# Performance work log

Measured on AMD Instinct MI355X. Metric: run time of the kernel, lower is better.

The kernel has to match this reference:

```python
import jax, jax.numpy as jnp
import numpy as np

LN_EPS = 1e-5


def _sage_mean(x, Wl, bl, src, dst, ew, n_nodes):
    # lin_l then gather-weight-scatter mean: out[i] = mean_{j->i} ew * (x[j] @ Wl + bl)
    h = x @ Wl + bl                                  # [N, D]
    msg = h[src] * ew[:, None]                       # [E, D] gather + scale
    s = jax.ops.segment_sum(msg, dst, num_segments=n_nodes)          # [N, D]
    cnt = jax.ops.segment_sum(jnp.ones_like(ew), dst, num_segments=n_nodes)
    return s / jnp.maximum(cnt, 1.0)[:, None]


def _layernorm(x, gamma, beta):
    mu = jnp.mean(x, axis=-1, keepdims=True)
    var = jnp.var(x, axis=-1, keepdims=True)
    return (x - mu) * jax.lax.rsqrt(var + LN_EPS) * gamma + beta


def setup_inputs() -> dict:
    key = jax.random.key(0)
    ks = jax.random.split(key, 8)
    N, E, D = 50000, 800000, 128
    x = jax.random.normal(ks[0], (N, D), dtype=jnp.float32)
    edge_index = jax.random.randint(ks[1], (2, E), 0, N, dtype=jnp.int64)
    edge_weight = jax.random.uniform(ks[2], (E,), dtype=jnp.float32)
    sc = 1.0 / np.sqrt(D)
    Wl1 = jax.random.normal(ks[3], (D, D), dtype=jnp.float32) * sc
    bl1 = jnp.zeros((D,), dtype=jnp.float32)
    Wl2 = jax.random.normal(ks[4], (D, D), dtype=jnp.float32) * sc
    bl2 = jnp.zeros((D,), dtype=jnp.float32)
    gamma = jnp.ones((D,), dtype=jnp.float32)
    beta = jnp.zeros((D,), dtype=jnp.float32)
    return {"x": x, "edge_index": edge_index, "edge_weight": edge_weight,
            "Wl1": Wl1, "bl1": bl1, "Wl2": Wl2, "bl2": bl2,
            "gamma": gamma, "beta": beta}


def reference(x, edge_index, edge_weight, Wl1, bl1, Wl2, bl2, gamma, beta):
    N = x.shape[0]
    src, dst = edge_index[0], edge_index[1]
    # Layer 1: WeightedSAGEConv (no self-loops; update() returns aggr only)
    x1 = _sage_mean(x, Wl1, bl1, src, dst, edge_weight, N)
    # Layer 2: ResGraphConv — residual is Identity (in==out), add self-loops w=1
    loops = jnp.arange(N, dtype=edge_index.dtype)
    src2 = jnp.concatenate([src, loops])
    dst2 = jnp.concatenate([dst, loops])
    ew2 = jnp.concatenate([edge_weight, jnp.ones((N,), dtype=edge_weight.dtype)])
    out = _sage_mean(x1, Wl2, bl2, src2, dst2, ew2, N)
    out = _layernorm(out + x1, gamma, beta)
    return jax.nn.gelu(out, approximate=False)
```

## Files before the change

kernel.cpp:

```cpp
#include <hip/hip_runtime.h>
#include <math.h>

#define DF 128
#define NPB 256
#define EPB 4096
#define CAP 7168

typedef __attribute__((ext_vector_type(8))) short bf16x8;
typedef __attribute__((ext_vector_type(4))) float f32x4;

__device__ __forceinline__ float bf2f(uint u) {
    union { uint i; float f; } v; v.i = u << 16; return v.f;
}
__device__ __forceinline__ uint f2bf(float f) {
    union { float f; uint i; } v; v.f = f;
    return (v.i + 0x7fffu + ((v.i >> 16) & 1u)) >> 16;
}


__global__ void prep_k(const float* __restrict__ x, uint* __restrict__ xb, int n4,
                       const float* __restrict__ W1, const float* __restrict__ W2,
                       uint* __restrict__ Wt1, uint* __restrict__ Wt2,
                       const int* __restrict__ dst, int* __restrict__ bhist, int E,
                       int cvtxB) {
    __shared__ int lh[256];
    int b = blockIdx.x;
    int t = threadIdx.x;
    if (b < cvtxB) {
        int i = b * 256 + t;
        if (i < n4) {
            float4 v = ((const float4*)x)[i];
            uint2 o;
            o.x = f2bf(v.x) | (f2bf(v.y) << 16);
            o.y = f2bf(v.z) | (f2bf(v.w) << 16);
            ((uint2*)xb)[i] = o;
        }
    } else if (b < cvtxB + 64) {
        int i = (b - cvtxB) * 256 + t;
        const float* W = (i < 8192) ? W1 : W2;
        uint* Wt = (i < 8192) ? Wt1 : Wt2;
        int j = i & 8191;
        int n = j >> 6, kk = j & 63;
        Wt[n * 64 + kk] = f2bf(W[(2 * kk) * DF + n]) | (f2bf(W[(2 * kk + 1) * DF + n]) << 16);
    } else {
        int hb = b - cvtxB - 64;
        int base = hb * EPB;
        lh[t] = 0;
        __syncthreads();
#pragma unroll
        for (int k = 0; k < EPB / 256; ++k) {
            int i = base + k * 256 + t;
            if (i < E) atomicAdd(&lh[dst[i] >> 8], 1);
        }
        __syncthreads();
        bhist[hb * 256 + t] = lh[t];
    }
}

__global__ void bscan_k(const int* __restrict__ bhist, int histB,
                        int* __restrict__ bkoff, int* __restrict__ gcur) {
    int t = threadIdx.x;
    int v = 0;
#pragma unroll 4
    for (int hb = 0; hb < histB; ++hb) v += bhist[hb * 256 + t];
    __shared__ int sm[256];
    sm[t] = v;
    __syncthreads();
    for (int off = 1; off < 256; off <<= 1) {
        int u = (t >= off) ? sm[t - off] : 0;
        __syncthreads();
        sm[t] += u;
        __syncthreads();
    }
    int ex = sm[t] - v;
    bkoff[t] = ex;
    gcur[t] = ex;
    if (t == 255) bkoff[256] = sm[255];
}

__global__ __launch_bounds__(256) void passA_k(
    const int* __restrict__ src, const int* __restrict__ dst,
    const float* __restrict__ ew, int* __restrict__ gcur,
    uint2* __restrict__ stage, int E) {
    __shared__ int lhist[256];
    __shared__ int lscan[256];
    __shared__ int lcur[256];
    __shared__ int gbase[256];
    __shared__ unsigned char lbk[EPB];
    __shared__ uint2 img[EPB];
    int t = threadIdx.x;
    int base = blockIdx.x * EPB;
    int cnt = min(EPB, E - base);
    lhist[t] = 0;
    __syncthreads();
    uint ps[16], pw[16];
    int pb[16];
#pragma unroll
    for (int k = 0; k < 16; ++k) {
        int i = base + k * 256 + t;
        pb[k] = -1;
        if (i < E) {
            int d = dst[i];
            int bk = d >> 8;
            pb[k] = bk;
            ps[k] = (uint)src[i] | ((uint)(d & 255) << 23);
            pw[k] = __float_as_uint(ew[i]);
            atomicAdd(&lhist[bk], 1);
        }
    }
    __syncthreads();
    int v = lhist[t];
    lscan[t] = v;
    __syncthreads();
    for (int off = 1; off < 256; off <<= 1) {
        int u = (t >= off) ? lscan[t - off] : 0;
        __syncthreads();
        lscan[t] += u;
        __syncthreads();
    }
    lcur[t] = lscan[t] - v;
    if (v > 0) gbase[t] = atomicAdd(&gcur[t], v);
    __syncthreads();
#pragma unroll
    for (int k = 0; k < 16; ++k) {
        if (pb[k] >= 0) {
            int p = atomicAdd(&lcur[pb[k]], 1);
            img[p] = make_uint2(ps[k], pw[k]);
            lbk[p] = (unsigned char)pb[k];
        }
    }
    __syncthreads();
    for (int i = t; i < cnt; i += 256) {
        int bk = lbk[i];
        stage[gbase[bk] + (i - (lscan[bk] - lhist[bk]))] = img[i];
    }
}

__global__ __launch_bounds__(256) void passB_k(
    const uint2* __restrict__ stage, const int* __restrict__ bkoff,
    int* __restrict__ rowptr, int* __restrict__ cursor,
    int2* __restrict__ adj, int N, int nbk) {
    __shared__ int lhist[256];
    __shared__ int lpre[256];
    __shared__ int lcur[256];
    __shared__ uint2 img[CAP];
    int t = threadIdx.x;
    int b = blockIdx.x;
    int nb0 = b * NPB;
    int nn = min(NPB, N - nb0);
    int ebase = bkoff[b];
    int ecnt = bkoff[b + 1] - ebase;
    lhist[t] = 0;
    __syncthreads();
    for (int i = t; i < ecnt; i += 256) {
        uint2 e = stage[ebase + i];
        atomicAdd(&lhist[(e.x >> 23) & 255], 1);
    }
    __syncthreads();
    int v = lhist[t];
    lpre[t] = v;
    __syncthreads();
    for (int off = 1; off < 256; off <<= 1) {
        int u = (t >= off) ? lpre[t - off] : 0;
        __syncthreads();
        lpre[t] += u;
        __syncthreads();
    }
    int myoff = lpre[t] - v;
    lcur[t] = myoff;
    if (t < nn) {
        rowptr[nb0 + t] = ebase + myoff;
        cursor[nb0 + t] = ebase + myoff;
    }
    if (b == nbk - 1 && t == 0) rowptr[N] = ebase + ecnt;
    __syncthreads();
    if (ecnt <= CAP) {
        for (int i = t; i < ecnt; i += 256) {
            uint2 e = stage[ebase + i];
            int p = atomicAdd(&lcur[(e.x >> 23) & 255], 1);
            img[p] = make_uint2(e.x & 0x7fffffu, e.y);
        }
        __syncthreads();
        for (int i = t; i < ecnt; i += 256) {
            uint2 e = img[i];
            adj[ebase + i] = make_int2((int)e.x, (int)e.y);
        }
    } else {
        for (int i = t; i < ecnt; i += 256) {
            uint2 e = stage[ebase + i];
            int dl = (e.x >> 23) & 255;
            int p = atomicAdd(&cursor[nb0 + dl], 1);
            adj[p] = make_int2((int)(e.x & 0x7fffffu), (int)e.y);
        }
    }
}


__global__ void histn_k(const int* __restrict__ dst, int* __restrict__ cnt, int E) {
    int i = blockIdx.x * blockDim.x + threadIdx.x;
    if (i < E) atomicAdd(&cnt[dst[i]], 1);
}

__global__ void partial_k(const int* __restrict__ cnt, int* __restrict__ bsum, int N) {
    int t = threadIdx.x, b = blockIdx.x;
    int base = b * 1024 + t * 4;
    int s = 0;
    if (base + 4 <= N) {
        int4 v = *(const int4*)(cnt + base);
        s = v.x + v.y + v.z + v.w;
    } else {
        for (int j = 0; j < 4; ++j)
            if (base + j < N) s += cnt[base + j];
    }
    __shared__ int sm[256];
    sm[t] = s;
    __syncthreads();
    for (int off = 128; off > 0; off >>= 1) {
        if (t < off) sm[t] += sm[t + off];
        __syncthreads();
    }
    if (t == 0) bsum[b] = sm[0];
}

__global__ void scanb_k(const int* __restrict__ bsum, int* __restrict__ boff,
                        int* __restrict__ rowptr, int nb, int N) {
    int t = threadIdx.x;
    int v = (t < nb) ? bsum[t] : 0;
    __shared__ int sm[256];
    sm[t] = v;
    __syncthreads();
    for (int off = 1; off < 256; off <<= 1) {
        int u = (t >= off) ? sm[t - off] : 0;
        __syncthreads();
        sm[t] += u;
        __syncthreads();
    }
    if (t < nb) boff[t] = sm[t] - v;
    if (t == 255) rowptr[N] = sm[255];
}

__global__ void rowfill_k(const int* __restrict__ cnt, const int* __restrict__ boff,
                          int* __restrict__ rowptr, int* __restrict__ cursor, int N) {
    int t = threadIdx.x, b = blockIdx.x;
    int base = b * 1024 + t * 4;
    int c0 = 0, c1 = 0, c2 = 0, c3 = 0;
    if (base + 4 <= N) {
        int4 v = *(const int4*)(cnt + base);
        c0 = v.x; c1 = v.y; c2 = v.z; c3 = v.w;
    } else {
        if (base + 0 < N) c0 = cnt[base + 0];
        if (base + 1 < N) c1 = cnt[base + 1];
        if (base + 2 < N) c2 = cnt[base + 2];
        if (base + 3 < N) c3 = cnt[base + 3];
    }
    int s = c0 + c1 + c2 + c3;
    __shared__ int sm[256];
    sm[t] = s;
    __syncthreads();
    for (int off = 1; off < 256; off <<= 1) {
        int u = (t >= off) ? sm[t - off] : 0;
        __syncthreads();
        sm[t] += u;
        __syncthreads();
    }
    int run = boff[b] + sm[t] - s;
    if (base + 0 < N) { rowptr[base + 0] = run; cursor[base + 0] = run; run += c0; }
    if (base + 1 < N) { rowptr[base + 1] = run; cursor[base + 1] = run; run += c1; }
    if (base + 2 < N) { rowptr[base + 2] = run; cursor[base + 2] = run; run += c2; }
    if (base + 3 < N) { rowptr[base + 3] = run; cursor[base + 3] = run; run += c3; }
}

__global__ void fill_k(const int* __restrict__ src, const int* __restrict__ dst,
                       const float* __restrict__ ew, int* __restrict__ cursor,
                       int2* __restrict__ adj, int E) {
    int i = blockIdx.x * blockDim.x + threadIdx.x;
    if (i < E) {
        int p = atomicAdd(&cursor[dst[i]], 1);
        int2 e;
        e.x = src[i];
        e.y = __float_as_int(ew[i]);
        adj[p] = e;
    }
}


template <int SELF>
__global__ void agg_k(const uint2* __restrict__ xb2, const int* __restrict__ rowptr,
                      const int2* __restrict__ adj, uint2* __restrict__ aggb2,
                      float* __restrict__ sumew, int N) {
    int wid = (blockIdx.x * blockDim.x + threadIdx.x) >> 6;
    int lane = threadIdx.x & 63;
    if (wid >= N) return;
    int half = lane >> 5;
    int sl = lane & 31;
    int lo = rowptr[wid], hi = rowptr[wid + 1];
    float a0 = 0.f, a1 = 0.f, a2 = 0.f, a3 = 0.f, ws = 0.f;
    if (SELF && half == 0) {
        uint2 v = xb2[(size_t)wid * 32 + sl];
        a0 = bf2f(v.x & 0xffffu); a1 = bf2f(v.x >> 16);
        a2 = bf2f(v.y & 0xffffu); a3 = bf2f(v.y >> 16);
    }
    for (int base = lo; base < hi; base += 64) {
        int p = base + lane;
        int sidx = 0; float wv = 0.f;
        if (p < hi) {
            int2 e = adj[p];
            sidx = e.x;
            wv = __int_as_float(e.y);
        }
        ws += wv;
        int cnt = min(hi - base, 64);
        int j = 0;
        for (; j + 8 <= cnt; j += 8) {
            int s0 = __shfl(sidx, j + half),     s1 = __shfl(sidx, j + 2 + half);
            int s2 = __shfl(sidx, j + 4 + half), s3 = __shfl(sidx, j + 6 + half);
            float w0 = __shfl(wv, j + half),     w1 = __shfl(wv, j + 2 + half);
            float w2 = __shfl(wv, j + 4 + half), w3 = __shfl(wv, j + 6 + half);
            uint2 v0 = xb2[(size_t)s0 * 32 + sl];
            uint2 v1 = xb2[(size_t)s1 * 32 + sl];
            uint2 v2 = xb2[(size_t)s2 * 32 + sl];
            uint2 v3 = xb2[(size_t)s3 * 32 + sl];
            a0 += w0 * bf2f(v0.x & 0xffffu); a1 += w0 * bf2f(v0.x >> 16);
            a2 += w0 * bf2f(v0.y & 0xffffu); a3 += w0 * bf2f(v0.y >> 16);
            a0 += w1 * bf2f(v1.x & 0xffffu); a1 += w1 * bf2f(v1.x >> 16);
            a2 += w1 * bf2f(v1.y & 0xffffu); a3 += w1 * bf2f(v1.y >> 16);
            a0 += w2 * bf2f(v2.x & 0xffffu); a1 += w2 * bf2f(v2.x >> 16);
            a2 += w2 * bf2f(v2.y & 0xffffu); a3 += w2 * bf2f(v2.y >> 16);
            a0 += w3 * bf2f(v3.x & 0xffffu); a1 += w3 * bf2f(v3.x >> 16);
            a2 += w3 * bf2f(v3.y & 0xffffu); a3 += w3 * bf2f(v3.y >> 16);
        }
        for (; j < cnt; j += 2) {
            int s0 = __shfl(sidx, j + half);
            float w0 = __shfl(wv, j + half);
            uint2 v0 = xb2[(size_t)s0 * 32 + sl];
            a0 += w0 * bf2f(v0.x & 0xffffu); a1 += w0 * bf2f(v0.x >> 16);
            a2 += w0 * bf2f(v0.y & 0xffffu); a3 += w0 * bf2f(v0.y >> 16);
        }
    }
    a0 += __shfl_xor(a0, 32);
    a1 += __shfl_xor(a1, 32);
    a2 += __shfl_xor(a2, 32);
    a3 += __shfl_xor(a3, 32);
    if (!SELF) {
        ws += __shfl_xor(ws, 1);
        ws += __shfl_xor(ws, 2);
        ws += __shfl_xor(ws, 4);
        ws += __shfl_xor(ws, 8);
        ws += __shfl_xor(ws, 16);
        ws += __shfl_xor(ws, 32);
        if (lane == 0) sumew[wid] = ws;
    }
    float inv = SELF ? 1.0f / (float)(hi - lo + 1)
                     : 1.0f / fmaxf((float)(hi - lo), 1.0f);
    if (half == 0) {
        uint2 o;
        o.x = f2bf(a0 * inv) | (f2bf(a1 * inv) << 16);
        o.y = f2bf(a2 * inv) | (f2bf(a3 * inv) << 16);
        aggb2[(size_t)wid * 32 + sl] = o;
    }
}


__global__ __launch_bounds__(256) void mm1_k(
    const ushort* __restrict__ aggb, const ushort* __restrict__ Wt,
    const float* __restrict__ bl, const float* __restrict__ sumew,
    const int* __restrict__ rowptr, ushort* __restrict__ x1b, int N) {
    int lane = threadIdx.x & 63;
    int strip = blockIdx.x * 4 + (threadIdx.x >> 6);
    int nstrips = (N + 15) >> 4;
    if (strip >= nstrips) return;
    int row0 = strip << 4;
    int arow = row0 + (lane & 15);
    if (arow >= N) arow = N - 1;
    int kg = (lane >> 4) << 3;
    int bcol = lane & 15;

    bf16x8 af[4];
#pragma unroll
    for (int kc = 0; kc < 4; ++kc)
        af[kc] = *(const bf16x8*)(aggb + (size_t)arow * DF + kc * 32 + kg);

    f32x4 acc[8];
#pragma unroll
    for (int nt = 0; nt < 8; ++nt) {
        f32x4 a = {0.f, 0.f, 0.f, 0.f};
#pragma unroll
        for (int kc = 0; kc < 4; ++kc) {
            bf16x8 bf = *(const bf16x8*)(Wt + (size_t)(nt * 16 + bcol) * DF + kc * 32 + kg);
            a = __builtin_amdgcn_mfma_f32_16x16x32_bf16(af[kc], bf, a, 0, 0, 0);
        }
        acc[nt] = a;
    }

#pragma unroll
    for (int r = 0; r < 4; ++r) {
        int R = row0 + ((lane >> 4) << 2) + r;
        if (R >= N) continue;
        int deg = rowptr[R + 1] - rowptr[R];
        float wb = sumew[R] / fmaxf((float)deg, 1.0f);
#pragma unroll
        for (int nt = 0; nt < 8; ++nt) {
            int col = nt * 16 + bcol;
            x1b[(size_t)R * DF + col] = (ushort)f2bf(acc[nt][r] + bl[col] * wb);
        }
    }
}

__device__ __forceinline__ float gelu_exact(float v) {
    return 0.5f * v * (1.0f + erff(v * 0.70710678118654752440f));
}

__global__ __launch_bounds__(256) void mm2_k(
    const ushort* __restrict__ aggb, const ushort* __restrict__ Wt,
    const float* __restrict__ bl, const float* __restrict__ sumew,
    const int* __restrict__ rowptr, const ushort* __restrict__ x1b,
    const float* __restrict__ gamma, const float* __restrict__ beta,
    float* __restrict__ out, int N) {
    int lane = threadIdx.x & 63;
    int strip = blockIdx.x * 4 + (threadIdx.x >> 6);
    int nstrips = (N + 15) >> 4;
    if (strip >= nstrips) return;
    int row0 = strip << 4;
    int arow = row0 + (lane & 15);
    if (arow >= N) arow = N - 1;
    int kg = (lane >> 4) << 3;
    int bcol = lane & 15;

    bf16x8 af[4];
#pragma unroll
    for (int kc = 0; kc < 4; ++kc)
        af[kc] = *(const bf16x8*)(aggb + (size_t)arow * DF + kc * 32 + kg);

    f32x4 acc[8];
#pragma unroll
    for (int nt = 0; nt < 8; ++nt) {
        f32x4 a = {0.f, 0.f, 0.f, 0.f};
#pragma unroll
        for (int kc = 0; kc < 4; ++kc) {
            bf16x8 bf = *(const bf16x8*)(Wt + (size_t)(nt * 16 + bcol) * DF + kc * 32 + kg);
            a = __builtin_amdgcn_mfma_f32_16x16x32_bf16(af[kc], bf, a, 0, 0, 0);
        }
        acc[nt] = a;
    }

#pragma unroll
    for (int r = 0; r < 4; ++r) {
        int R = row0 + ((lane >> 4) << 2) + r;
        if (R >= N) continue;
        int deg = rowptr[R + 1] - rowptr[R];
        float wb = (sumew[R] + 1.0f) / (float)(deg + 1);
        float pre[8];
        float s = 0.f;
#pragma unroll
        for (int nt = 0; nt < 8; ++nt) {
            int col = nt * 16 + bcol;
            pre[nt] = acc[nt][r] + bl[col] * wb + bf2f(x1b[(size_t)R * DF + col]);
            s += pre[nt];
        }
        s += __shfl_xor(s, 1);
        s += __shfl_xor(s, 2);
        s += __shfl_xor(s, 4);
        s += __shfl_xor(s, 8);
        float mu = s * (1.0f / 128.0f);
        float vs = 0.f;
#pragma unroll
        for (int nt = 0; nt < 8; ++nt) {
            float d = pre[nt] - mu;
            vs += d * d;
        }
        vs += __shfl_xor(vs, 1);
        vs += __shfl_xor(vs, 2);
        vs += __shfl_xor(vs, 4);
        vs += __shfl_xor(vs, 8);
        float rstd = rsqrtf(vs * (1.0f / 128.0f) + 1e-5f);
#pragma unroll
        for (int nt = 0; nt < 8; ++nt) {
            int col = nt * 16 + bcol;
            float y = (pre[nt] - mu) * rstd * gamma[col] + beta[col];
            out[(size_t)R * DF + col] = gelu_exact(y);
        }
    }
}


extern "C" void kernel_launch(void* const* d_in, const int* in_sizes, int n_in,
                              void* d_out, int out_size, void* d_ws, size_t ws_size,
                              hipStream_t stream) {
    const float* x     = (const float*)d_in[0];
    const int*   ei    = (const int*)d_in[1];
    const float* ew    = (const float*)d_in[2];
    const float* Wl1   = (const float*)d_in[3];
    const float* bl1   = (const float*)d_in[4];
    const float* Wl2   = (const float*)d_in[5];
    const float* bl2   = (const float*)d_in[6];
    const float* gamma = (const float*)d_in[7];
    const float* beta  = (const float*)d_in[8];
    float* out = (float*)d_out;

    int N = in_sizes[0] / DF;
    int E = in_sizes[2];
    const int* src = ei;
    const int* dst = ei + E;

    char* ws = (char*)d_ws;
    size_t off = 0;
    auto alloc = [&](size_t bytes) -> void* {
        void* p = ws + off;
        off += (bytes + 255) & ~(size_t)255;
        return p;
    };
    int histB = (E + EPB - 1) / EPB;
    float*  sumew   = (float*)alloc((size_t)N * 4);
    int*    rowptr  = (int*)alloc((size_t)(N + 1) * 4);
    int*    cursor  = (int*)alloc((size_t)N * 4);
    int*    bhist   = (int*)alloc((size_t)histB * 256 * 4);
    int*    bkoff   = (int*)alloc(1040);
    int*    gcur    = (int*)alloc(1024);
    int*    bsum    = (int*)alloc(1024);
    int*    boff    = (int*)alloc(1024);
    int2*   adj     = (int2*)alloc((size_t)E * 8);
    uint2*  stage   = (uint2*)alloc((size_t)E * 8);
    uint*   xb      = (uint*)alloc((size_t)N * DF * 2);
    uint*   aggb    = (uint*)alloc((size_t)N * DF * 2);
    ushort* x1b     = (ushort*)alloc((size_t)N * DF * 2);
    uint*   Wt1     = (uint*)alloc((size_t)DF * DF * 2);
    uint*   Wt2     = (uint*)alloc((size_t)DF * DF * 2);
    int*    cnt     = (int*)alloc((size_t)N * 4);

    int nbk = (N + NPB - 1) / NPB;
    int n4 = N * DF / 4;
    int cvtxB = (n4 + 255) / 256;

    if (nbk <= 256) {
        hipLaunchKernelGGL(prep_k, dim3(cvtxB + 64 + histB), dim3(256), 0, stream,
                           x, xb, n4, Wl1, Wl2, Wt1, Wt2, dst, bhist, E, cvtxB);
        hipLaunchKernelGGL(bscan_k, dim3(1), dim3(256), 0, stream, bhist, histB, bkoff, gcur);
        hipLaunchKernelGGL(passA_k, dim3(histB), dim3(256), 0, stream, src, dst, ew, gcur, stage, E);
        hipLaunchKernelGGL(passB_k, dim3(nbk), dim3(256), 0, stream,
                           stage, bkoff, rowptr, cursor, adj, N, nbk);
    } else {
        hipMemsetAsync(cnt, 0, (size_t)N * 4, stream);
        hipLaunchKernelGGL(prep_k, dim3(cvtxB + 64), dim3(256), 0, stream,
                           x, xb, n4, Wl1, Wl2, Wt1, Wt2, dst, bhist, 0, cvtxB);
        int eb = (E + 255) / 256;
        hipLaunchKernelGGL(histn_k, dim3(eb), dim3(256), 0, stream, dst, cnt, E);
        int nb_scan = (N + 1023) / 1024;
        hipLaunchKernelGGL(partial_k, dim3(nb_scan), dim3(256), 0, stream, cnt, bsum, N);
        hipLaunchKernelGGL(scanb_k, dim3(1), dim3(256), 0, stream, bsum, boff, rowptr, nb_scan, N);
        hipLaunchKernelGGL(rowfill_k, dim3(nb_scan), dim3(256), 0, stream, cnt, boff, rowptr, cursor, N);
        hipLaunchKernelGGL(fill_k, dim3(eb), dim3(256), 0, stream, src, dst, ew, cursor, adj, E);
    }

    int nb = (N * 64 + 255) / 256;
    int nstrips = (N + 15) / 16;
    int mb = (nstrips + 3) / 4;

    hipLaunchKernelGGL(agg_k<0>, dim3(nb), dim3(256), 0, stream,
                       (const uint2*)xb, rowptr, adj, (uint2*)aggb, sumew, N);
    hipLaunchKernelGGL(mm1_k, dim3(mb), dim3(256), 0, stream,
                       (const ushort*)aggb, (const ushort*)Wt1, bl1, sumew, rowptr, x1b, N);
    hipLaunchKernelGGL(agg_k<1>, dim3(nb), dim3(256), 0, stream,
                       (const uint2*)x1b, rowptr, adj, (uint2*)aggb, sumew, N);
    hipLaunchKernelGGL(mm2_k, dim3(mb), dim3(256), 0, stream,
                       (const ushort*)aggb, (const ushort*)Wt2, bl2, sumew, rowptr, x1b, gamma, beta, out, N);
}
```

Measured before the change: 167.8 us.

## Fold bucket scan into passA and deepen gather unrolling in aggregation

Removes the single-block bscan kernel. Each passA block now reads the full per-block histogram table, computes the global bucket scan redundantly plus its own prefix, and derives deterministic global offsets instead of using atomics on gcur. This drops one launch and the serial single-block step, at the cost of every block reading histB×256 ints. The SpMM gather loop also now issues 8 independent row loads per half-wave before accumulating, to raise memory-level parallelism.

```diff
diff --git a/kernel.cpp b/kernel.cpp
--- a/kernel.cpp
+++ b/kernel.cpp
@@ -57,42 +57,22 @@
     }
 }
 
-__global__ void bscan_k(const int* __restrict__ bhist, int histB,
-                        int* __restrict__ bkoff, int* __restrict__ gcur) {
-    int t = threadIdx.x;
-    int v = 0;
-#pragma unroll 4
-    for (int hb = 0; hb < histB; ++hb) v += bhist[hb * 256 + t];
-    __shared__ int sm[256];
-    sm[t] = v;
-    __syncthreads();
-    for (int off = 1; off < 256; off <<= 1) {
-        int u = (t >= off) ? sm[t - off] : 0;
-        __syncthreads();
-        sm[t] += u;
-        __syncthreads();
-    }
-    int ex = sm[t] - v;
-    bkoff[t] = ex;
-    gcur[t] = ex;
-    if (t == 255) bkoff[256] = sm[255];
-}
-
 __global__ __launch_bounds__(256) void passA_k(
     const int* __restrict__ src, const int* __restrict__ dst,
-    const float* __restrict__ ew, int* __restrict__ gcur,
-    uint2* __restrict__ stage, int E) {
+    const float* __restrict__ ew, const int* __restrict__ bhist, int histB,
+    int* __restrict__ bkoff, uint2* __restrict__ stage, int E) {
     __shared__ int lhist[256];
     __shared__ int lscan[256];
     __shared__ int lcur[256];
     __shared__ int gbase[256];
+    __shared__ int sm[256];
     __shared__ unsigned char lbk[EPB];
     __shared__ uint2 img[EPB];
     int t = threadIdx.x;
-    int base = blockIdx.x * EPB;
+    int hb = blockIdx.x;
+    int base = hb * EPB;
     int cnt = min(EPB, E - base);
-    lhist[t] = 0;
-    __syncthreads();
+
     uint ps[16], pw[16];
     int pb[16];
 #pragma unroll
@@ -101,26 +81,47 @@
         pb[k] = -1;
         if (i < E) {
             int d = dst[i];
-            int bk = d >> 8;
-            pb[k] = bk;
+            pb[k] = d >> 8;
             ps[k] = (uint)src[i] | ((uint)(d & 255) << 23);
             pw[k] = __float_as_uint(ew[i]);
-            atomicAdd(&lhist[bk], 1);
-        }
-    }
-    __syncthreads();
-    int v = lhist[t];
-    lscan[t] = v;
+        }
+    }
+
+    int colsum = 0, pre = 0, own = 0;
+    for (int h = 0; h < histB; ++h) {
+        int v = bhist[h * 256 + t];
+        colsum += v;
+        if (h < hb) pre += v;
+        if (h == hb) own = v;
+    }
+    sm[t] = colsum;
     __syncthreads();
     for (int off = 1; off < 256; off <<= 1) {
-        int u = (t >= off) ? lscan[t - off] : 0;
-        __syncthreads();
-        lscan[t] += u;
-        __syncthreads();
-    }
-    lcur[t] = lscan[t] - v;
-    if (v > 0) gbase[t] = atomicAdd(&gcur[t], v);
-    __syncthreads();
+        int u = (t >= off) ? sm[t - off] : 0;
+        __syncthreads();
+        sm[t] += u;
+        __syncthreads();
+    }
+    int bkx = sm[t] - colsum;
+    gbase[t] = bkx + pre;
+    if (hb == 0) {
+        bkoff[t] = bkx;
+        if (t == 255) bkoff[256] = sm[255];
+    }
+    __syncthreads();
+    sm[t] = own;
+    __syncthreads();
+    for (int off = 1; off < 256; off <<= 1) {
+        int u = (t >= off) ? sm[t - off] : 0;
+        __syncthreads();
+        sm[t] += u;
+        __syncthreads();
+    }
+    lhist[t] = own;
+    lscan[t] = sm[t];
+    lcur[t] = sm[t] - own;
+    __syncthreads();
+
 #pragma unroll
     for (int k = 0; k < 16; ++k) {
         if (pb[k] >= 0) {
@@ -311,23 +312,30 @@
         ws += wv;
         int cnt = min(hi - base, 64);
         int j = 0;
-        for (; j + 8 <= cnt; j += 8) {
-            int s0 = __shfl(sidx, j + half),     s1 = __shfl(sidx, j + 2 + half);
-            int s2 = __shfl(sidx, j + 4 + half), s3 = __shfl(sidx, j + 6 + half);
-            float w0 = __shfl(wv, j + half),     w1 = __shfl(wv, j + 2 + half);
-            float w2 = __shfl(wv, j + 4 + half), w3 = __shfl(wv, j + 6 + half);
+        for (; j + 16 <= cnt; j += 16) {
+            int ss[8]; float ww[8]; uint2 vv[8];
+#pragma unroll
+            for (int q = 0; q < 8; ++q) {
+                ss[q] = __shfl(sidx, j + 2 * q + half);
+                ww[q] = __shfl(wv, j + 2 * q + half);
+            }
+#pragma unroll
+            for (int q = 0; q < 8; ++q) vv[q] = xb2[(size_t)ss[q] * 32 + sl];
+#pragma unroll
+            for (int q = 0; q < 8; ++q) {
+                a0 += ww[q] * bf2f(vv[q].x & 0xffffu); a1 += ww[q] * bf2f(vv[q].x >> 16);
+                a2 += ww[q] * bf2f(vv[q].y & 0xffffu); a3 += ww[q] * bf2f(vv[q].y >> 16);
+            }
+        }
+        for (; j + 4 <= cnt; j += 4) {
+            int s0 = __shfl(sidx, j + half), s1 = __shfl(sidx, j + 2 + half);
+            float w0 = __shfl(wv, j + half), w1 = __shfl(wv, j + 2 + half);
             uint2 v0 = xb2[(size_t)s0 * 32 + sl];
             uint2 v1 = xb2[(size_t)s1 * 32 + sl];
-            uint2 v2 = xb2[(size_t)s2 * 32 + sl];
-            uint2 v3 = xb2[(size_t)s3 * 32 + sl];
             a0 += w0 * bf2f(v0.x & 0xffffu); a1 += w0 * bf2f(v0.x >> 16);
             a2 += w0 * bf2f(v0.y & 0xffffu); a3 += w0 * bf2f(v0.y >> 16);
             a0 += w1 * bf2f(v1.x & 0xffffu); a1 += w1 * bf2f(v1.x >> 16);
             a2 += w1 * bf2f(v1.y & 0xffffu); a3 += w1 * bf2f(v1.y >> 16);
-            a0 += w2 * bf2f(v2.x & 0xffffu); a1 += w2 * bf2f(v2.x >> 16);
-            a2 += w2 * bf2f(v2.y & 0xffffu); a3 += w2 * bf2f(v2.y >> 16);
-            a0 += w3 * bf2f(v3.x & 0xffffu); a1 += w3 * bf2f(v3.x >> 16);
-            a2 += w3 * bf2f(v3.y & 0xffffu); a3 += w3 * bf2f(v3.y >> 16);
         }
         for (; j < cnt; j += 2) {
             int s0 = __shfl(sidx, j + half);
@@ -515,7 +523,6 @@
     int*    cursor  = (int*)alloc((size_t)N * 4);
     int*    bhist   = (int*)alloc((size_t)histB * 256 * 4);
     int*    bkoff   = (int*)alloc(1040);
-    int*    gcur    = (int*)alloc(1024);
     int*    bsum    = (int*)alloc(1024);
     int*    boff    = (int*)alloc(1024);
     int2*   adj     = (int2*)alloc((size_t)E * 8);
@@ -534,8 +541,8 @@
     if (nbk <= 256) {
         hipLaunchKernelGGL(prep_k, dim3(cvtxB + 64 + histB), dim3(256), 0, stream,
                            x, xb, n4, Wl1, Wl2, Wt1, Wt2, dst, bhist, E, cvtxB);
-        hipLaunchKernelGGL(bscan_k, dim3(1), dim3(256), 0, stream, bhist, histB, bkoff, gcur);
-        hipLaunchKernelGGL(passA_k, dim3(histB), dim3(256), 0, stream, src, dst, ew, gcur, stage, E);
+        hipLaunchKernelGGL(passA_k, dim3(histB), dim3(256), 0, stream,
+                           src, dst, ew, bhist, histB, bkoff, stage, E);
         hipLaunchKernelGGL(passB_k, dim3(nbk), dim3(256), 0, stream,
                            stage, bkoff, rowptr, cursor, adj, N, nbk);
     } else {
```

After: 200.1 us. 19.3% more time.
